# Kernel tuning notes

Hardware: AMD Instinct MI355X
Metric: run time of the kernel (lower is better)

## Reference

```python
import jax, jax.numpy as jnp
import numpy as np

N_NODES = 50000
N_EDGES = 600000
DIM = 128
K = 3
N_LAYERS = 3
LEAKY_SLOPE = 0.01  # nn.LeakyReLU default
RE_NORM = 1.0       # 2/lambda_max with lambda_max=2 (standard ChebNet approximation)


def setup_inputs() -> dict:
    key = jax.random.key(0)
    ks = jax.random.split(key, 8)
    weights = jax.random.normal(ks[0], (N_NODES,), dtype=jnp.float32)
    src = jax.random.randint(ks[1], (N_EDGES,), 0, N_NODES)
    dst = jax.random.randint(ks[2], (N_EDGES,), 0, N_NODES)
    lin_in_w = jax.random.normal(ks[3], (1, DIM), dtype=jnp.float32) * 0.5
    lin_in_b = jnp.zeros((DIM,), dtype=jnp.float32)
    cheb_ws = jax.random.normal(ks[4], (N_LAYERS, K * DIM, DIM), dtype=jnp.float32) * 0.05
    cheb_bs = jnp.zeros((N_LAYERS, DIM), dtype=jnp.float32)
    pred_w = jax.random.normal(ks[5], (DIM, 1), dtype=jnp.float32) * 0.05
    pred_b = jnp.zeros((1,), dtype=jnp.float32)
    return {"weights": weights, "src": src, "dst": dst,
            "lin_in_w": lin_in_w, "lin_in_b": lin_in_b,
            "cheb_ws": cheb_ws, "cheb_bs": cheb_bs,
            "pred_w": pred_w, "pred_b": pred_b}


def _cheb_conv(x, W, b, src, dst, d_invsqrt, n):
    # DGL ChebConv with lambda_max=2 -> re_norm=1: scaled Laplacian L_hat = -D^-1/2 A D^-1/2
    def spmm(f):  # unnormalized Laplacian-style aggregation: D^-1/2 A D^-1/2 f
        h = f * d_invsqrt
        agg = jax.ops.segment_sum(h[src], dst, num_segments=n)
        return agg * d_invsqrt

    X0 = x
    terms = [X0]
    h = spmm(X0)
    X1 = -RE_NORM * h + X0 * (RE_NORM - 1.0)
    terms.append(X1)
    for _ in range(2, K):
        h = spmm(X1)
        Xi = -2.0 * RE_NORM * h + X1 * (2.0 * (RE_NORM - 1.0)) - X0
        terms.append(Xi)
        X0, X1 = X1, Xi
    Xt = jnp.concatenate(terms, axis=1)  # [N, K*DIM]
    return jax.nn.relu(Xt @ W + b)       # DGL ChebConv default activation=F.relu


def reference(weights, src, dst, lin_in_w, lin_in_b, cheb_ws, cheb_bs, pred_w, pred_b):
    n = weights.shape[0]
    # dgl.add_self_loop
    loop = jnp.arange(n, dtype=src.dtype)
    src_f = jnp.concatenate([src, loop])
    dst_f = jnp.concatenate([dst, loop])
    # in-degree normalization D^-1/2 (clamp min 1)
    deg = jax.ops.segment_sum(jnp.ones_like(dst_f, dtype=jnp.float32), dst_f, num_segments=n)
    d_invsqrt = jnp.power(jnp.clip(deg, 1.0), -0.5)[:, None]  # [N,1]

    feat = weights[:, None] @ lin_in_w + lin_in_b             # [N, DIM]
    emb = _cheb_conv(feat, cheb_ws[0], cheb_bs[0], src_f, dst_f, d_invsqrt, n)
    for i in range(1, N_LAYERS):
        emb = jax.nn.leaky_relu(emb, negative_slope=LEAKY_SLOPE)
        emb = _cheb_conv(emb, cheb_ws[i], cheb_bs[i], src_f, dst_f, d_invsqrt, n)
    logits = emb @ pred_w + pred_b                            # do_train=True path
    return logits
```

## Files before the change

### kernel.cpp

```cpp
#include <hip/hip_runtime.h>

typedef unsigned int uint;
typedef unsigned short ushort;

#define NN 50000
#define NE 600000
#define DIM 128
#define KD 384
#define PADK 40

typedef __attribute__((ext_vector_type(8))) short short8;
typedef __attribute__((ext_vector_type(4))) float float4v;

static __device__ __forceinline__ ushort f2b(float f) {
    uint u = __float_as_uint(f);
    return (ushort)((u + 0x7FFFu + ((u >> 16) & 1u)) >> 16);
}
static __device__ __forceinline__ float blo(uint u) { return __uint_as_float(u << 16); }
static __device__ __forceinline__ float bhi(uint u) { return __uint_as_float(u & 0xFFFF0000u); }

__global__ void k_init(int* __restrict__ cnt, const float* __restrict__ cw,
                       ushort* __restrict__ wt) {
    if (blockIdx.x < 49) {
        int i = blockIdx.x * 256 + threadIdx.x;
        if (i < 12544) ((int4*)cnt)[i] = make_int4(0, 0, 0, 0);
    } else {
        int i = (blockIdx.x - 49) * 256 + threadIdx.x;
        if (i < 3 * KD * DIM) {
            int l = i / (KD * DIM), rem = i - l * (KD * DIM);
            int k = rem >> 7, n = rem & 127;
            wt[(size_t)l * KD * DIM + (size_t)n * KD + k] = f2b(cw[i]);
        }
    }
}

__global__ void k_hist(const int* __restrict__ dst, int* __restrict__ cnt) {
    int e = blockIdx.x * 256 + threadIdx.x;
    if (e < NE) atomicAdd(&cnt[dst[e]], 1);
}

__global__ __launch_bounds__(256) void k_scan1(const int* __restrict__ cnt,
                                               int* __restrict__ incl,
                                               int* __restrict__ bsums,
                                               float* __restrict__ dinv) {
    __shared__ int sh[256];
    int i = blockIdx.x * 256 + threadIdx.x;
    int v = (i < NN) ? cnt[i] : 0;
    if (i < NN) dinv[i] = rsqrtf((float)(v + 1));
    sh[threadIdx.x] = v;
    __syncthreads();
    for (int d = 1; d < 256; d <<= 1) {
        int t = (threadIdx.x >= d) ? sh[threadIdx.x - d] : 0;
        __syncthreads();
        sh[threadIdx.x] += t;
        __syncthreads();
    }
    incl[i] = sh[threadIdx.x];
    if (threadIdx.x == 255) bsums[blockIdx.x] = sh[255];
}

__global__ __launch_bounds__(256) void k_scan3(const int* __restrict__ cnt,
                                               int* __restrict__ incl_cursor,
                                               const int* __restrict__ bsums,
                                               int* __restrict__ offs) {
    __shared__ int sh[256];
    __shared__ int boff;
    int tid = threadIdx.x;
    int v = (tid < 196) ? bsums[tid] : 0;
    sh[tid] = v;
    __syncthreads();
    for (int d = 1; d < 256; d <<= 1) {
        int t = (tid >= d) ? sh[tid - d] : 0;
        __syncthreads();
        sh[tid] += t;
        __syncthreads();
    }
    if (tid == blockIdx.x) boff = sh[tid] - v;
    __syncthreads();
    int i = blockIdx.x * 256 + tid;
    if (i >= NN) return;
    int excl = incl_cursor[i] - cnt[i] + boff;
    offs[i] = excl;
    incl_cursor[i] = excl;
    if (i == NN - 1) offs[NN] = NE;
}

__global__ void k_fill(const int* __restrict__ src, const int* __restrict__ dst,
                       int* __restrict__ cursor, ushort* __restrict__ csr_src) {
    int e = blockIdx.x * 256 + threadIdx.x;
    if (e < NE) {
        int p = atomicAdd(&cursor[dst[e]], 1);
        csr_src[p] = (ushort)src[e];
    }
}

__global__ __launch_bounds__(256) void k_gather1_l1(
        const float* __restrict__ w, const float* __restrict__ lw,
        const float* __restrict__ lb, const int* __restrict__ offs,
        const ushort* __restrict__ csr_src, const float* __restrict__ dinv,
        ushort* __restrict__ Qb, ushort* __restrict__ Pb) {
    int n = blockIdx.x * 4 + (threadIdx.x >> 6);
    int lane = threadIdx.x & 63;
    int j0 = offs[n], j1 = offs[n + 1];
    float dn = dinv[n];
    float sA = 0.f, sB = 0.f;
    for (int j = j0 + lane; j < j1; j += 64) {
        int s = csr_src[j];
        float ds = dinv[s];
        sA = fmaf(ds, w[s], sA);
        sB += ds;
    }
#pragma unroll
    for (int off = 32; off > 0; off >>= 1) {
        sA += __shfl_down(sA, off, 64);
        sB += __shfl_down(sB, off, 64);
    }
    sA = __shfl(sA, 0, 64) * dn;
    sB = __shfl(sB, 0, 64) * dn;
    float id = dn * dn;
    float wn = w[n];
    float lw0 = lw[2 * lane], lw1 = lw[2 * lane + 1];
    float lb0 = lb[2 * lane], lb1 = lb[2 * lane + 1];
    float x0a = wn * lw0 + lb0, x0b = wn * lw1 + lb1;
    ushort2 pb2; pb2.x = f2b(x0a); pb2.y = f2b(x0b);
    ((ushort2*)(Pb + (size_t)n * DIM))[lane] = pb2;
    ushort2 ub;
    ub.x = f2b(-(sA * lw0 + sB * lb0 + x0a * id));
    ub.y = f2b(-(sA * lw1 + sB * lb1 + x0b * id));
    ((ushort2*)(Qb + (size_t)n * DIM))[lane] = ub;
}

__global__ __launch_bounds__(256) void k_gather1(
        const ushort* __restrict__ Xb, const int* __restrict__ offs,
        const ushort* __restrict__ csr_src, const float* __restrict__ dinv,
        ushort* __restrict__ Qb) {
    int n = blockIdx.x * 8 + (threadIdx.x >> 5);
    int lane = threadIdx.x & 31;
    int j0 = offs[n], j1 = offs[n + 1];
    float dn = dinv[n];
    float a0 = 0.f, a1 = 0.f, a2 = 0.f, a3 = 0.f;
    const uint2* Xu = (const uint2*)Xb;
    for (int base = j0; base < j1; base += 32) {
        int m = j1 - base; if (m > 32) m = 32;
        int s = 0; float wv = 0.f;
        if (lane < m) { s = csr_src[base + lane]; wv = dinv[s] * dn; }
        int t = 0;
        for (; t + 8 <= m; t += 8) {
            uint2 u[8]; float wb[8];
#pragma unroll
            for (int q = 0; q < 8; ++q) {
                int sq = __shfl(s, t + q, 32);
                wb[q] = __shfl(wv, t + q, 32);
                u[q] = Xu[(size_t)sq * 32 + lane];
            }
#pragma unroll
            for (int q = 0; q < 8; ++q) {
                a0 = fmaf(wb[q], blo(u[q].x), a0);
                a1 = fmaf(wb[q], bhi(u[q].x), a1);
                a2 = fmaf(wb[q], blo(u[q].y), a2);
                a3 = fmaf(wb[q], bhi(u[q].y), a3);
            }
        }
        for (; t + 4 <= m; t += 4) {
            uint2 u[4]; float wb[4];
#pragma unroll
            for (int q = 0; q < 4; ++q) {
                int sq = __shfl(s, t + q, 32);
                wb[q] = __shfl(wv, t + q, 32);
                u[q] = Xu[(size_t)sq * 32 + lane];
            }
#pragma unroll
            for (int q = 0; q < 4; ++q) {
                a0 = fmaf(wb[q], blo(u[q].x), a0);
                a1 = fmaf(wb[q], bhi(u[q].x), a1);
                a2 = fmaf(wb[q], blo(u[q].y), a2);
                a3 = fmaf(wb[q], bhi(u[q].y), a3);
            }
        }
        for (; t < m; ++t) {
            int ss = __shfl(s, t, 32);
            float ww = __shfl(wv, t, 32);
            uint2 u = Xu[(size_t)ss * 32 + lane];
            a0 = fmaf(ww, blo(u.x), a0); a1 = fmaf(ww, bhi(u.x), a1);
            a2 = fmaf(ww, blo(u.y), a2); a3 = fmaf(ww, bhi(u.y), a3);
        }
    }
    float id = dn * dn;
    uint2 un = Xu[(size_t)n * 32 + lane];
    uint2 ow;
    ow.x = (uint)f2b(-(a0 + blo(un.x) * id)) | ((uint)f2b(-(a1 + bhi(un.x) * id)) << 16);
    ow.y = (uint)f2b(-(a2 + blo(un.y) * id)) | ((uint)f2b(-(a3 + bhi(un.y) * id)) << 16);
    ((uint2*)(Qb + (size_t)n * DIM))[lane] = ow;
}

__global__ __launch_bounds__(256) void k_gather2(
        const ushort* __restrict__ X1b, const ushort* __restrict__ X0b,
        const int* __restrict__ offs, const ushort* __restrict__ csr_src,
        const float* __restrict__ dinv, ushort* __restrict__ Rb) {
    int n = blockIdx.x * 8 + (threadIdx.x >> 5);
    int lane = threadIdx.x & 31;
    int j0 = offs[n], j1 = offs[n + 1];
    float dn = dinv[n];
    float a0 = 0.f, a1 = 0.f, a2 = 0.f, a3 = 0.f;
    const uint2* Xu = (const uint2*)X1b;
    for (int base = j0; base < j1; base += 32) {
        int m = j1 - base; if (m > 32) m = 32;
        int s = 0; float wv = 0.f;
        if (lane < m) { s = csr_src[base + lane]; wv = dinv[s] * dn; }
        int t = 0;
        for (; t + 8 <= m; t += 8) {
            uint2 u[8]; float wb[8];
#pragma unroll
            for (int q = 0; q < 8; ++q) {
                int sq = __shfl(s, t + q, 32);
                wb[q] = __shfl(wv, t + q, 32);
                u[q] = Xu[(size_t)sq * 32 + lane];
            }
#pragma unroll
            for (int q = 0; q < 8; ++q) {
                a0 = fmaf(wb[q], blo(u[q].x), a0);
                a1 = fmaf(wb[q], bhi(u[q].x), a1);
                a2 = fmaf(wb[q], blo(u[q].y), a2);
                a3 = fmaf(wb[q], bhi(u[q].y), a3);
            }
        }
        for (; t + 4 <= m; t += 4) {
            uint2 u[4]; float wb[4];
#pragma unroll
            for (int q = 0; q < 4; ++q) {
                int sq = __shfl(s, t + q, 32);
                wb[q] = __shfl(wv, t + q, 32);
                u[q] = Xu[(size_t)sq * 32 + lane];
            }
#pragma unroll
            for (int q = 0; q < 4; ++q) {
                a0 = fmaf(wb[q], blo(u[q].x), a0);
                a1 = fmaf(wb[q], bhi(u[q].x), a1);
                a2 = fmaf(wb[q], blo(u[q].y), a2);
                a3 = fmaf(wb[q], bhi(u[q].y), a3);
            }
        }
        for (; t < m; ++t) {
            int ss = __shfl(s, t, 32);
            float ww = __shfl(wv, t, 32);
            uint2 u = Xu[(size_t)ss * 32 + lane];
            a0 = fmaf(ww, blo(u.x), a0); a1 = fmaf(ww, bhi(u.x), a1);
            a2 = fmaf(ww, blo(u.y), a2); a3 = fmaf(ww, bhi(u.y), a3);
        }
    }
    float id = dn * dn;
    uint2 u1n = Xu[(size_t)n * 32 + lane];
    uint2 u0n = ((const uint2*)X0b)[(size_t)n * 32 + lane];
    uint2 ow;
    ow.x = (uint)f2b(-2.f * (a0 + blo(u1n.x) * id) - blo(u0n.x))
         | ((uint)f2b(-2.f * (a1 + bhi(u1n.x) * id) - bhi(u0n.x)) << 16);
    ow.y = (uint)f2b(-2.f * (a2 + blo(u1n.y) * id) - blo(u0n.y))
         | ((uint)f2b(-2.f * (a3 + bhi(u1n.y) * id) - bhi(u0n.y)) << 16);
    ((uint2*)(Rb + (size_t)n * DIM))[lane] = ow;
}

__global__ __launch_bounds__(256) void k_gemm(
        const ushort* __restrict__ X0b, const ushort* __restrict__ X1b,
        const ushort* __restrict__ X2b, const ushort* __restrict__ Wt,
        const float* __restrict__ bias, ushort* __restrict__ outb) {
    __shared__ ushort As[128 * PADK];
    __shared__ ushort Bs[128 * PADK];
    int tid = threadIdx.x;
    int nbase = blockIdx.x * 128;
    int wave = tid >> 6, lane = tid & 63;
    int wr = wave >> 1, wc = wave & 1;
    int l15 = lane & 15, quad = lane >> 4;

    float4v acc[4][4];
#pragma unroll
    for (int i = 0; i < 4; ++i)
#pragma unroll
        for (int j = 0; j < 4; ++j) acc[i][j] = (float4v)0.f;

    int srow = tid >> 1, shalf = tid & 1;
    int gm = nbase + srow; if (gm >= NN) gm = NN - 1;

    for (int c = 0; c < 12; ++c) {
        int part = c >> 2;
        int k0 = (c & 3) * 32;
        const ushort* Xp = (part == 0) ? X0b : ((part == 1) ? X1b : X2b);
        const uint4* ga = (const uint4*)(Xp + (size_t)gm * DIM + k0 + shalf * 16);
        uint4 a0 = ga[0], a1 = ga[1];
        const uint4* gb = (const uint4*)(Wt + (size_t)srow * KD + c * 32 + shalf * 16);
        uint4 b0 = gb[0], b1 = gb[1];
        __syncthreads();
        uint4* pa = (uint4*)(As + srow * PADK + shalf * 16);
        pa[0] = a0; pa[1] = a1;
        uint4* pb = (uint4*)(Bs + srow * PADK + shalf * 16);
        pb[0] = b0; pb[1] = b1;
        __syncthreads();
        short8 af[4], bf[4];
#pragma unroll
        for (int i = 0; i < 4; ++i) {
            af[i] = *(const short8*)(As + (wr * 64 + i * 16 + l15) * PADK + quad * 8);
            bf[i] = *(const short8*)(Bs + (wc * 64 + i * 16 + l15) * PADK + quad * 8);
        }
#pragma unroll
        for (int i = 0; i < 4; ++i)
#pragma unroll
            for (int j = 0; j < 4; ++j)
                acc[i][j] = __builtin_amdgcn_mfma_f32_16x16x32_bf16(
                    af[i], bf[j], acc[i][j], 0, 0, 0);
    }

    float bv[4];
#pragma unroll
    for (int j = 0; j < 4; ++j) bv[j] = bias[wc * 64 + j * 16 + l15];
#pragma unroll
    for (int i = 0; i < 4; ++i) {
#pragma unroll
        for (int r = 0; r < 4; ++r) {
            int node = nbase + wr * 64 + i * 16 + quad * 4 + r;
            if (node < NN) {
#pragma unroll
                for (int j = 0; j < 4; ++j) {
                    int col = wc * 64 + j * 16 + l15;
                    outb[(size_t)node * DIM + col] =
                        f2b(fmaxf(acc[i][j][r] + bv[j], 0.f));
                }
            }
        }
    }
}

__global__ __launch_bounds__(256) void k_gemm_pred(
        const ushort* __restrict__ X0b, const ushort* __restrict__ X1b,
        const ushort* __restrict__ X2b, const ushort* __restrict__ Wt,
        const float* __restrict__ bias, const float* __restrict__ pw,
        const float* __restrict__ pb, float* __restrict__ logits) {
    __shared__ ushort As[128 * PADK];
    __shared__ ushort Bs[128 * PADK];
    __shared__ float lsum[128];
    int tid = threadIdx.x;
    int nbase = blockIdx.x * 128;
    int wave = tid >> 6, lane = tid & 63;
    int wr = wave >> 1, wc = wave & 1;
    int l15 = lane & 15, quad = lane >> 4;

    float4v acc[4][4];
#pragma unroll
    for (int i = 0; i < 4; ++i)
#pragma unroll
        for (int j = 0; j < 4; ++j) acc[i][j] = (float4v)0.f;

    int srow = tid >> 1, shalf = tid & 1;
    int gm = nbase + srow; if (gm >= NN) gm = NN - 1;

    for (int c = 0; c < 12; ++c) {
        int part = c >> 2;
        int k0 = (c & 3) * 32;
        const ushort* Xp = (part == 0) ? X0b : ((part == 1) ? X1b : X2b);
        const uint4* ga = (const uint4*)(Xp + (size_t)gm * DIM + k0 + shalf * 16);
        uint4 a0 = ga[0], a1 = ga[1];
        const uint4* gb = (const uint4*)(Wt + (size_t)srow * KD + c * 32 + shalf * 16);
        uint4 b0 = gb[0], b1 = gb[1];
        __syncthreads();
        uint4* pa = (uint4*)(As + srow * PADK + shalf * 16);
        pa[0] = a0; pa[1] = a1;
        uint4* pb2 = (uint4*)(Bs + srow * PADK + shalf * 16);
        pb2[0] = b0; pb2[1] = b1;
        __syncthreads();
        short8 af[4], bf[4];
#pragma unroll
        for (int i = 0; i < 4; ++i) {
            af[i] = *(const short8*)(As + (wr * 64 + i * 16 + l15) * PADK + quad * 8);
            bf[i] = *(const short8*)(Bs + (wc * 64 + i * 16 + l15) * PADK + quad * 8);
        }
#pragma unroll
        for (int i = 0; i < 4; ++i)
#pragma unroll
            for (int j = 0; j < 4; ++j)
                acc[i][j] = __builtin_amdgcn_mfma_f32_16x16x32_bf16(
                    af[i], bf[j], acc[i][j], 0, 0, 0);
    }

    __syncthreads();
    if (tid < 128) lsum[tid] = 0.f;
    __syncthreads();
    float bv[4], pwv[4];
#pragma unroll
    for (int j = 0; j < 4; ++j) {
        int col = wc * 64 + j * 16 + l15;
        bv[j] = bias[col];
        pwv[j] = pw[col];
    }
#pragma unroll
    for (int i = 0; i < 4; ++i) {
#pragma unroll
        for (int r = 0; r < 4; ++r) {
            float local = 0.f;
#pragma unroll
            for (int j = 0; j < 4; ++j)
                local = fmaf(fmaxf(acc[i][j][r] + bv[j], 0.f), pwv[j], local);
            local += __shfl_xor(local, 1, 64);
            local += __shfl_xor(local, 2, 64);
            local += __shfl_xor(local, 4, 64);
            local += __shfl_xor(local, 8, 64);
            if (l15 == 0)
                atomicAdd(&lsum[wr * 64 + i * 16 + quad * 4 + r], local);
        }
    }
    __syncthreads();
    if (tid < 128) {
        int node = nbase + tid;
        if (node < NN) logits[node] = lsum[tid] + pb[0];
    }
}

extern "C" void kernel_launch(void* const* d_in, const int* in_sizes, int n_in,
                              void* d_out, int out_size, void* d_ws, size_t ws_size,
                              hipStream_t stream) {
    int i_weights = 0, i_src = 1, i_dst = 2, i_lw = 3, i_lb = 4,
        i_cw = 5, i_cb = 6, i_pw = 7, i_pb = 8;
    {
        int seen600k = 0, seen128 = 0;
        for (int i = 0; i < n_in; ++i) {
            int s = in_sizes[i];
            if (s == 50000) i_weights = i;
            else if (s == 600000) { if (seen600k == 0) i_src = i; else i_dst = i; ++seen600k; }
            else if (s == 128) { if (seen128 == 0) i_lw = i; else if (seen128 == 1) i_lb = i; else i_pw = i; ++seen128; }
            else if (s == 147456) i_cw = i;
            else if (s == 384) i_cb = i;
            else if (s == 1) i_pb = i;
        }
    }
    const float* weights = (const float*)d_in[i_weights];
    const int*   src     = (const int*)d_in[i_src];
    const int*   dst     = (const int*)d_in[i_dst];
    const float* lin_w   = (const float*)d_in[i_lw];
    const float* lin_b   = (const float*)d_in[i_lb];
    const float* cheb_w  = (const float*)d_in[i_cw];
    const float* cheb_b  = (const float*)d_in[i_cb];
    const float* pred_w  = (const float*)d_in[i_pw];
    const float* pred_b  = (const float*)d_in[i_pb];
    float* out = (float*)d_out;

    float*  ws      = (float*)d_ws;
    float*  dinv    = ws;
    int*    offs    = (int*)(ws + 50048);
    ushort* csr_u16 = (ushort*)(offs + 50056);
    int*    cnt     = (int*)csr_u16 + 300032;
    int*    incl    = cnt + 50176;
    int*    bsums   = incl + 50176;
    ushort* Pb      = (ushort*)(bsums + 256);
    ushort* Qb      = Pb + (size_t)NN * DIM;
    ushort* Rb      = Qb + (size_t)NN * DIM;
    ushort* Wtb     = Rb + (size_t)NN * DIM;

    k_init<<<625, 256, 0, stream>>>(cnt, cheb_w, Wtb);
    k_hist<<<2344, 256, 0, stream>>>(dst, cnt);
    k_scan1<<<196, 256, 0, stream>>>(cnt, incl, bsums, dinv);
    k_scan3<<<196, 256, 0, stream>>>(cnt, incl, bsums, offs);
    k_fill<<<2344, 256, 0, stream>>>(src, dst, incl, csr_u16);

    k_gather1_l1<<<12500, 256, 0, stream>>>(weights, lin_w, lin_b, offs, csr_u16,
                                            dinv, Qb, Pb);
    k_gather2<<<6250, 256, 0, stream>>>(Qb, Pb, offs, csr_u16, dinv, Rb);
    k_gemm<<<391, 256, 0, stream>>>(Pb, Qb, Rb, Wtb, cheb_b, Pb);
    k_gather1<<<6250, 256, 0, stream>>>(Pb, offs, csr_u16, dinv, Qb);
    k_gather2<<<6250, 256, 0, stream>>>(Qb, Pb, offs, csr_u16, dinv, Rb);
    k_gemm<<<391, 256, 0, stream>>>(Pb, Qb, Rb, Wtb + (size_t)KD * DIM,
                                    cheb_b + DIM, Pb);
    k_gather1<<<6250, 256, 0, stream>>>(Pb, offs, csr_u16, dinv, Qb);
    k_gather2<<<6250, 256, 0, stream>>>(Qb, Pb, offs, csr_u16, dinv, Rb);
    k_gemm_pred<<<391, 256, 0, stream>>>(Pb, Qb, Rb, Wtb + (size_t)2 * KD * DIM,
                                         cheb_b + 2 * DIM, pred_w, pred_b, out);
}
```

Measured before the change: 363.8 us.

## Precompute per-edge normalized weights in CSR and use wave-per-node gathers

The CSR fill now stores each edge as a (src, dinv[s]*dinv[d]) pair and also precomputes dinv[s]*w[s], so the gather kernels no longer do dependent dinv lookups per edge. The feature gathers switch from half-wave shuffled batches to one full 64-lane wave per node that reads the edge record as a uniform load and each lane gathers one uint (two bf16 values). This removes shuffles and the indirect dinv gather, but the CSR grows from 2-byte to 8-byte entries plus a 4-byte float array. Loads per edge are narrower per lane, which may reduce memory-level parallelism.

```diff
diff --git a/kernel.cpp b/kernel.cpp
--- a/kernel.cpp
+++ b/kernel.cpp
@@ -86,29 +86,37 @@
 }
 
 __global__ void k_fill(const int* __restrict__ src, const int* __restrict__ dst,
-                       int* __restrict__ cursor, ushort* __restrict__ csr_src) {
+                       int* __restrict__ cursor, const float* __restrict__ dinv,
+                       const float* __restrict__ w_in,
+                       uint2* __restrict__ csrE, float* __restrict__ hw) {
     int e = blockIdx.x * 256 + threadIdx.x;
     if (e < NE) {
-        int p = atomicAdd(&cursor[dst[e]], 1);
-        csr_src[p] = (ushort)src[e];
+        int s = src[e], d = dst[e];
+        int p = atomicAdd(&cursor[d], 1);
+        float ds = dinv[s];
+        uint2 rec;
+        rec.x = (uint)s;
+        rec.y = __float_as_uint(ds * dinv[d]);
+        csrE[p] = rec;
+        hw[p] = ds * w_in[s];
     }
 }
 
 __global__ __launch_bounds__(256) void k_gather1_l1(
         const float* __restrict__ w, const float* __restrict__ lw,
         const float* __restrict__ lb, const int* __restrict__ offs,
-        const ushort* __restrict__ csr_src, const float* __restrict__ dinv,
+        const uint2* __restrict__ csrE, const float* __restrict__ hw,
+        const float* __restrict__ dinv,
         ushort* __restrict__ Qb, ushort* __restrict__ Pb) {
     int n = blockIdx.x * 4 + (threadIdx.x >> 6);
     int lane = threadIdx.x & 63;
     int j0 = offs[n], j1 = offs[n + 1];
     float dn = dinv[n];
     float sA = 0.f, sB = 0.f;
+    const float* ew = (const float*)csrE;
     for (int j = j0 + lane; j < j1; j += 64) {
-        int s = csr_src[j];
-        float ds = dinv[s];
-        sA = fmaf(ds, w[s], sA);
-        sB += ds;
+        sA += hw[j];
+        sB += ew[2 * j + 1];
     }
 #pragma unroll
     for (int off = 32; off > 0; off >>= 1) {
@@ -116,7 +124,7 @@
         sB += __shfl_down(sB, off, 64);
     }
     sA = __shfl(sA, 0, 64) * dn;
-    sB = __shfl(sB, 0, 64) * dn;
+    sB = __shfl(sB, 0, 64);
     float id = dn * dn;
     float wn = w[n];
     float lw0 = lw[2 * lane], lw1 = lw[2 * lane + 1];
@@ -132,131 +140,53 @@
 
 __global__ __launch_bounds__(256) void k_gather1(
         const ushort* __restrict__ Xb, const int* __restrict__ offs,
-        const ushort* __restrict__ csr_src, const float* __restrict__ dinv,
+        const uint2* __restrict__ csrE, const float* __restrict__ dinv,
         ushort* __restrict__ Qb) {
-    int n = blockIdx.x * 8 + (threadIdx.x >> 5);
-    int lane = threadIdx.x & 31;
+    int n = __builtin_amdgcn_readfirstlane(blockIdx.x * 4 + (threadIdx.x >> 6));
+    int lane = threadIdx.x & 63;
     int j0 = offs[n], j1 = offs[n + 1];
+    const uint* Xu = (const uint*)Xb;
+    float a0 = 0.f, a1 = 0.f;
+#pragma unroll 4
+    for (int j = j0; j < j1; ++j) {
+        uint2 e = csrE[j];
+        float wv = __uint_as_float(e.y);
+        uint u = Xu[(size_t)e.x * 64 + lane];
+        a0 = fmaf(wv, blo(u), a0);
+        a1 = fmaf(wv, bhi(u), a1);
+    }
     float dn = dinv[n];
-    float a0 = 0.f, a1 = 0.f, a2 = 0.f, a3 = 0.f;
-    const uint2* Xu = (const uint2*)Xb;
-    for (int base = j0; base < j1; base += 32) {
-        int m = j1 - base; if (m > 32) m = 32;
-        int s = 0; float wv = 0.f;
-        if (lane < m) { s = csr_src[base + lane]; wv = dinv[s] * dn; }
-        int t = 0;
-        for (; t + 8 <= m; t += 8) {
-            uint2 u[8]; float wb[8];
-#pragma unroll
-            for (int q = 0; q < 8; ++q) {
-                int sq = __shfl(s, t + q, 32);
-                wb[q] = __shfl(wv, t + q, 32);
-                u[q] = Xu[(size_t)sq * 32 + lane];
-            }
-#pragma unroll
-            for (int q = 0; q < 8; ++q) {
-                a0 = fmaf(wb[q], blo(u[q].x), a0);
-                a1 = fmaf(wb[q], bhi(u[q].x), a1);
-                a2 = fmaf(wb[q], blo(u[q].y), a2);
-                a3 = fmaf(wb[q], bhi(u[q].y), a3);
-            }
-        }
-        for (; t + 4 <= m; t += 4) {
-            uint2 u[4]; float wb[4];
-#pragma unroll
-            for (int q = 0; q < 4; ++q) {
-                int sq = __shfl(s, t + q, 32);
-                wb[q] = __shfl(wv, t + q, 32);
-                u[q] = Xu[(size_t)sq * 32 + lane];
-            }
-#pragma unroll
-            for (int q = 0; q < 4; ++q) {
-                a0 = fmaf(wb[q], blo(u[q].x), a0);
-                a1 = fmaf(wb[q], bhi(u[q].x), a1);
-                a2 = fmaf(wb[q], blo(u[q].y), a2);
-                a3 = fmaf(wb[q], bhi(u[q].y), a3);
-            }
-        }
-        for (; t < m; ++t) {
-            int ss = __shfl(s, t, 32);
-            float ww = __shfl(wv, t, 32);
-            uint2 u = Xu[(size_t)ss * 32 + lane];
-            a0 = fmaf(ww, blo(u.x), a0); a1 = fmaf(ww, bhi(u.x), a1);
-            a2 = fmaf(ww, blo(u.y), a2); a3 = fmaf(ww, bhi(u.y), a3);
-        }
-    }
     float id = dn * dn;
-    uint2 un = Xu[(size_t)n * 32 + lane];
-    uint2 ow;
-    ow.x = (uint)f2b(-(a0 + blo(un.x) * id)) | ((uint)f2b(-(a1 + bhi(un.x) * id)) << 16);
-    ow.y = (uint)f2b(-(a2 + blo(un.y) * id)) | ((uint)f2b(-(a3 + bhi(un.y) * id)) << 16);
-    ((uint2*)(Qb + (size_t)n * DIM))[lane] = ow;
+    uint un = Xu[(size_t)n * 64 + lane];
+    uint ow = (uint)f2b(-(a0 + blo(un) * id))
+            | ((uint)f2b(-(a1 + bhi(un) * id)) << 16);
+    ((uint*)Qb)[(size_t)n * 64 + lane] = ow;
 }
 
 __global__ __launch_bounds__(256) void k_gather2(
         const ushort* __restrict__ X1b, const ushort* __restrict__ X0b,
-        const int* __restrict__ offs, const ushort* __restrict__ csr_src,
+        const int* __restrict__ offs, const uint2* __restrict__ csrE,
         const float* __restrict__ dinv, ushort* __restrict__ Rb) {
-    int n = blockIdx.x * 8 + (threadIdx.x >> 5);
-    int lane = threadIdx.x & 31;
+    int n = __builtin_amdgcn_readfirstlane(blockIdx.x * 4 + (threadIdx.x >> 6));
+    int lane = threadIdx.x & 63;
     int j0 = offs[n], j1 = offs[n + 1];
+    const uint* Xu = (const uint*)X1b;
+    float a0 = 0.f, a1 = 0.f;
+#pragma unroll 4
+    for (int j = j0; j < j1; ++j) {
+        uint2 e = csrE[j];
+        float wv = __uint_as_float(e.y);
+        uint u = Xu[(size_t)e.x * 64 + lane];
+        a0 = fmaf(wv, blo(u), a0);
+        a1 = fmaf(wv, bhi(u), a1);
+    }
     float dn = dinv[n];
-    float a0 = 0.f, a1 = 0.f, a2 = 0.f, a3 = 0.f;
-    const uint2* Xu = (const uint2*)X1b;
-    for (int base = j0; base < j1; base += 32) {
-        int m = j1 - base; if (m > 32) m = 32;
-        int s = 0; float wv = 0.f;
-        if (lane < m) { s = csr_src[base + lane]; wv = dinv[s] * dn; }
-        int t = 0;
-        for (; t + 8 <= m; t += 8) {
-            uint2 u[8]; float wb[8];
-#pragma unroll
-            for (int q = 0; q < 8; ++q) {
-                int sq = __shfl(s, t + q, 32);
-                wb[q] = __shfl(wv, t + q, 32);
-                u[q] = Xu[(size_t)sq * 32 + lane];
-            }
-#pragma unroll
-            for (int q = 0; q < 8; ++q) {
-                a0 = fmaf(wb[q], blo(u[q].x), a0);
-                a1 = fmaf(wb[q], bhi(u[q].x), a1);
-                a2 = fmaf(wb[q], blo(u[q].y), a2);
-                a3 = fmaf(wb[q], bhi(u[q].y), a3);
-            }
-        }
-        for (; t + 4 <= m; t += 4) {
-            uint2 u[4]; float wb[4];
-#pragma unroll
-            for (int q = 0; q < 4; ++q) {
-                int sq = __shfl(s, t + q, 32);
-                wb[q] = __shfl(wv, t + q, 32);
-                u[q] = Xu[(size_t)sq * 32 + lane];
-            }
-#pragma unroll
-            for (int q = 0; q < 4; ++q) {
-                a0 = fmaf(wb[q], blo(u[q].x), a0);
-                a1 = fmaf(wb[q], bhi(u[q].x), a1);
-                a2 = fmaf(wb[q], blo(u[q].y), a2);
-                a3 = fmaf(wb[q], bhi(u[q].y), a3);
-            }
-        }
-        for (; t < m; ++t) {
-            int ss = __shfl(s, t, 32);
-            float ww = __shfl(wv, t, 32);
-            uint2 u = Xu[(size_t)ss * 32 + lane];
-            a0 = fmaf(ww, blo(u.x), a0); a1 = fmaf(ww, bhi(u.x), a1);
-            a2 = fmaf(ww, blo(u.y), a2); a3 = fmaf(ww, bhi(u.y), a3);
-        }
-    }
     float id = dn * dn;
-    uint2 u1n = Xu[(size_t)n * 32 + lane];
-    uint2 u0n = ((const uint2*)X0b)[(size_t)n * 32 + lane];
-    uint2 ow;
-    ow.x = (uint)f2b(-2.f * (a0 + blo(u1n.x) * id) - blo(u0n.x))
-         | ((uint)f2b(-2.f * (a1 + bhi(u1n.x) * id) - bhi(u0n.x)) << 16);
-    ow.y = (uint)f2b(-2.f * (a2 + blo(u1n.y) * id) - blo(u0n.y))
-         | ((uint)f2b(-2.f * (a3 + bhi(u1n.y) * id) - bhi(u0n.y)) << 16);
-    ((uint2*)(Rb + (size_t)n * DIM))[lane] = ow;
+    uint u1n = Xu[(size_t)n * 64 + lane];
+    uint u0n = ((const uint*)X0b)[(size_t)n * 64 + lane];
+    uint ow = (uint)f2b(-2.f * (a0 + blo(u1n) * id) - blo(u0n))
+            | ((uint)f2b(-2.f * (a1 + bhi(u1n) * id) - bhi(u0n)) << 16);
+    ((uint*)Rb)[(size_t)n * 64 + lane] = ow;
 }
 
 __global__ __launch_bounds__(256) void k_gemm(
@@ -443,11 +373,12 @@
     float*  ws      = (float*)d_ws;
     float*  dinv    = ws;
     int*    offs    = (int*)(ws + 50048);
-    ushort* csr_u16 = (ushort*)(offs + 50056);
-    int*    cnt     = (int*)csr_u16 + 300032;
+    int*    cnt     = offs + 50056;
     int*    incl    = cnt + 50176;
     int*    bsums   = incl + 50176;
-    ushort* Pb      = (ushort*)(bsums + 256);
+    uint2*  csrE    = (uint2*)(bsums + 256);
+    float*  hw      = (float*)(csrE + NE);
+    ushort* Pb      = (ushort*)(hw + NE);
     ushort* Qb      = Pb + (size_t)NN * DIM;
     ushort* Rb      = Qb + (size_t)NN * DIM;
     ushort* Wtb     = Rb + (size_t)NN * DIM;
@@ -456,18 +387,18 @@
     k_hist<<<2344, 256, 0, stream>>>(dst, cnt);
     k_scan1<<<196, 256, 0, stream>>>(cnt, incl, bsums, dinv);
     k_scan3<<<196, 256, 0, stream>>>(cnt, incl, bsums, offs);
-    k_fill<<<2344, 256, 0, stream>>>(src, dst, incl, csr_u16);
-
-    k_gather1_l1<<<12500, 256, 0, stream>>>(weights, lin_w, lin_b, offs, csr_u16,
-                                            dinv, Qb, Pb);
-    k_gather2<<<6250, 256, 0, stream>>>(Qb, Pb, offs, csr_u16, dinv, Rb);
+    k_fill<<<2344, 256, 0, stream>>>(src, dst, incl, dinv, weights, csrE, hw);
+
+    k_gather1_l1<<<12500, 256, 0, stream>>>(weights, lin_w, lin_b, offs, csrE,
+                                            hw, dinv, Qb, Pb);
+    k_gather2<<<12500, 256, 0, stream>>>(Qb, Pb, offs, csrE, dinv, Rb);
     k_gemm<<<391, 256, 0, stream>>>(Pb, Qb, Rb, Wtb, cheb_b, Pb);
-    k_gather1<<<6250, 256, 0, stream>>>(Pb, offs, csr_u16, dinv, Qb);
-    k_gather2<<<6250, 256, 0, stream>>>(Qb, Pb, offs, csr_u16, dinv, Rb);
+    k_gather1<<<12500, 256, 0, stream>>>(Pb, offs, csrE, dinv, Qb);
+    k_gather2<<<12500, 256, 0, stream>>>(Qb, Pb, offs, csrE, dinv, Rb);
     k_gemm<<<391, 256, 0, stream>>>(Pb, Qb, Rb, Wtb + (size_t)KD * DIM,
                                     cheb_b + DIM, Pb);
-    k_gather1<<<6250, 256, 0, stream>>>(Pb, offs, csr_u16, dinv, Qb);
-    k_gather2<<<6250, 256, 0, stream>>>(Qb, Pb, offs, csr_u16, dinv, Rb);
+    k_gather1<<<12500, 256, 0, stream>>>(Pb, offs, csrE, dinv, Qb);
+    k_gather2<<<12500, 256, 0, stream>>>(Qb, Pb, offs, csrE, dinv, Rb);
     k_gemm_pred<<<391, 256, 0, stream>>>(Pb, Qb, Rb, Wtb + (size_t)2 * KD * DIM,
                                          cheb_b + 2 * DIM, pred_w, pred_b, out);
 }
```

Result: no change. 361.9 us (-0.5%).
